# Kernel tuning notes

Measured on AMD Instinct MI355X. Metric: run time of the kernel, lower is better.

The kernel has to match this reference:

```python
import jax, jax.numpy as jnp
import numpy as np

N = 4096; TD = 768; ID = 512; H = 256; NH = 4; HD = H // NH; NC = 3; E = 131072


def _gcn(x, w, b, src, dst, n):
    # GCNConv: add self loops, sym-normalize, aggregate at dst
    loop = jnp.arange(n)
    s = jnp.concatenate([src, loop])
    d = jnp.concatenate([dst, loop])
    deg = jax.ops.segment_sum(jnp.ones(s.shape[0], x.dtype), d, num_segments=n)
    dinv = jnp.where(deg > 0, jax.lax.rsqrt(deg), 0.0)
    norm = dinv[s] * dinv[d]                      # [E+N]
    h = x @ w                                     # [N,H] transform
    out = jax.ops.segment_sum(norm[:, None] * h[s], d, num_segments=n)
    return out + b


def setup_inputs() -> dict:
    key = jax.random.key(0)
    ks = jax.random.split(key, 20)
    p = lambda k, shp, sc: jax.random.normal(k, shp, jnp.float32) * sc
    inp = {
        "text_features": jax.random.normal(ks[0], (N, TD), jnp.float32),
        "image_features": jax.random.normal(ks[1], (N, ID), jnp.float32),
        "edge_index": jax.random.randint(ks[2], (2, E), 0, N, jnp.int32),
        "text_w": p(ks[3], (TD, H), 0.02), "text_b": jnp.zeros((H,), jnp.float32),
        "image_w": p(ks[4], (ID, H), 0.02), "image_b": jnp.zeros((H,), jnp.float32),
        "wq": p(ks[5], (H, H), 0.02), "bq": jnp.zeros((H,), jnp.float32),
        "wk": p(ks[6], (H, H), 0.02), "bk": jnp.zeros((H,), jnp.float32),
        "wv": p(ks[7], (H, H), 0.02), "bv": jnp.zeros((H,), jnp.float32),
        "wo": p(ks[8], (H, H), 0.02), "bo": jnp.zeros((H,), jnp.float32),
        "gcn1_w": p(ks[9], (H, H), 0.02), "gcn1_b": jnp.zeros((H,), jnp.float32),
        "gcn2_w": p(ks[10], (H, H), 0.02), "gcn2_b": jnp.zeros((H,), jnp.float32),
        "cls_w": p(ks[11], (H, NC), 0.02), "cls_b": jnp.zeros((NC,), jnp.float32),
    }
    return inp


def reference(text_features, image_features, edge_index,
              text_w, text_b, image_w, image_b,
              wq, bq, wk, bk, wv, bv, wo, bo,
              gcn1_w, gcn1_b, gcn2_w, gcn2_b, cls_w, cls_b):
    # fused linear+relu projections, then elementwise fuse of sum
    combined = (jax.nn.relu(text_features @ text_w + text_b)
                + jax.nn.relu(image_features @ image_w + image_b))  # [N,H]
    # MHA over all nodes (seq_len=N, batch=1)
    q = (combined @ wq + bq).reshape(N, NH, HD)
    k = (combined @ wk + bk).reshape(N, NH, HD)
    v = (combined @ wv + bv).reshape(N, NH, HD)
    scores = jnp.einsum('nhd,mhd->hnm', q, k) / jnp.sqrt(jnp.float32(HD))
    attn = jax.nn.softmax(scores, axis=-1)
    o = jnp.einsum('hnm,mhd->nhd', attn, v).reshape(N, H)
    attn_out = o @ wo + bo
    # two GCN layers
    src, dst = edge_index[0], edge_index[1]
    g1 = jax.nn.relu(_gcn(attn_out, gcn1_w, gcn1_b, src, dst, N))
    g2 = _gcn(g1, gcn2_w, gcn2_b, src, dst, N)
    return g2 @ cls_w + cls_b
```

## Files before the change

kernel.cpp:

```cpp
#include <hip/hip_runtime.h>
#include <hip/hip_bf16.h>

typedef unsigned short ushort;
typedef __attribute__((ext_vector_type(8))) short short8;
typedef __attribute__((ext_vector_type(4))) short short4v;
typedef __attribute__((ext_vector_type(4))) float f32x4;

constexpr int N_  = 4096;
constexpr int TD_ = 768;
constexpr int ID_ = 512;
constexpr int H_  = 256;
constexpr int HD_ = 64;
constexpr int E_  = 131072;
constexpr int SPLITS = 8;
constexpr float QSCALE = 0.125f * 1.44269504088896f;

#define MFMA16(a, b, c) __builtin_amdgcn_mfma_f32_16x16x32_bf16(a, b, c, 0, 0, 0)

__device__ inline ushort f2bf(float x) {
    union { float f; unsigned u; } v; v.f = x;
    unsigned r = v.u + 0x7fff + ((v.u >> 16) & 1);
    return (ushort)(r >> 16);
}
__device__ inline float bf2f(ushort x) {
    union { unsigned u; float f; } v; v.u = ((unsigned)x) << 16;
    return v.f;
}

__device__ inline void gl_lds16(const void* g, void* l) {
    __builtin_amdgcn_global_load_lds((const __attribute__((address_space(1))) unsigned int*)g,
                                     (__attribute__((address_space(3))) unsigned int*)l, 16, 0, 0);
}

__device__ inline void stage64(const ushort* g, long long strideEl, ushort* lds, int w, int l) {
    int r8 = l >> 3;
    int cc = (l & 7) ^ r8;
    #pragma unroll
    for (int p = 0; p < 2; p++) {
        int row = w * 16 + p * 8 + r8;
        gl_lds16(g + (long long)row * strideEl + cc * 8, lds + (w * 16 + p * 8) * 64);
    }
}
__device__ inline int swz(int row, int kOff) {
    return row * 64 + ((((kOff >> 3) ^ (row & 7))) << 3);
}


__global__ __launch_bounds__(256) void k_init(int* __restrict__ indeg, int* __restrict__ pos) {
    int i = blockIdx.x * 256 + threadIdx.x;
    indeg[i] = 0;
    pos[i] = 0;
}

__global__ __launch_bounds__(256) void k_count(const int* __restrict__ dst, int* __restrict__ indeg) {
    int e = blockIdx.x * 256 + threadIdx.x;
    atomicAdd(&indeg[dst[e]], 1);
}

__global__ __launch_bounds__(1024) void k_scan(const int* __restrict__ indeg, int* __restrict__ offs,
                                               float* __restrict__ dinv) {
    __shared__ int sums[1024];
    int t = threadIdx.x;
    int b = t * 4;
    int a0 = indeg[b], a1 = indeg[b + 1], a2 = indeg[b + 2], a3 = indeg[b + 3];
    int s = a0 + a1 + a2 + a3;
    sums[t] = s;
    __syncthreads();
    for (int off = 1; off < 1024; off <<= 1) {
        int vv = (t >= off) ? sums[t - off] : 0;
        __syncthreads();
        sums[t] += vv;
        __syncthreads();
    }
    int excl = sums[t] - s;
    offs[b]     = excl;
    offs[b + 1] = excl + a0;
    offs[b + 2] = excl + a0 + a1;
    offs[b + 3] = excl + a0 + a1 + a2;
    dinv[b]     = 1.f / sqrtf((float)(a0 + 1));
    dinv[b + 1] = 1.f / sqrtf((float)(a1 + 1));
    dinv[b + 2] = 1.f / sqrtf((float)(a2 + 1));
    dinv[b + 3] = 1.f / sqrtf((float)(a3 + 1));
}

__global__ __launch_bounds__(256) void k_scatter(const int* __restrict__ src, const int* __restrict__ dst,
                                                 const int* __restrict__ offs, const float* __restrict__ dinv,
                                                 int* __restrict__ pos, int* __restrict__ ssrc,
                                                 float* __restrict__ sw) {
    int e = blockIdx.x * 256 + threadIdx.x;
    int s = src[e], d = dst[e];
    int p = atomicAdd(&pos[d], 1);
    int idx = offs[d] + p;
    ssrc[idx] = s;
    sw[idx] = dinv[s] * dinv[d];
}


__global__ __launch_bounds__(256) void k_cvt_feat(const float* __restrict__ text, const float* __restrict__ img,
                                                  ushort* __restrict__ tb, ushort* __restrict__ ib) {
    size_t base = ((size_t)blockIdx.x * 256 + threadIdx.x) * 8;
    const float* src;
    ushort* dst;
    if (base < (size_t)N_ * TD_) { src = text + base; dst = tb + base; }
    else { src = img + (base - (size_t)N_ * TD_); dst = ib + (base - (size_t)N_ * TD_); }
    float4 x = *(const float4*)src;
    float4 y = *(const float4*)(src + 4);
    ushort o[8] = { f2bf(x.x), f2bf(x.y), f2bf(x.z), f2bf(x.w),
                    f2bf(y.x), f2bf(y.y), f2bf(y.z), f2bf(y.w) };
    *(short8*)dst = *(const short8*)o;
}

__global__ __launch_bounds__(256) void k_cvtw(const float* __restrict__ tw, const float* __restrict__ iw,
                                              const float* __restrict__ wq, const float* __restrict__ wk,
                                              const float* __restrict__ wv, const float* __restrict__ wo,
                                              const float* __restrict__ g1w, const float* __restrict__ g2w,
                                              ushort* __restrict__ twT, ushort* __restrict__ iwT,
                                              ushort* __restrict__ wqT, ushort* __restrict__ wkT,
                                              ushort* __restrict__ wvT, ushort* __restrict__ woT,
                                              ushort* __restrict__ g1wT, ushort* __restrict__ g2wT) {
    __shared__ float Ts[64][65];
    const int zz = blockIdx.z;
    const float* src; ushort* dst; int R;
    switch (zz) {
        case 0: src = tw;  dst = twT;  R = 768; break;
        case 1: src = iw;  dst = iwT;  R = 512; break;
        case 2: src = wq;  dst = wqT;  R = 256; break;
        case 3: src = wk;  dst = wkT;  R = 256; break;
        case 4: src = wv;  dst = wvT;  R = 256; break;
        case 5: src = wo;  dst = woT;  R = 256; break;
        case 6: src = g1w; dst = g1wT; R = 256; break;
        default: src = g2w; dst = g2wT; R = 256; break;
    }
    const int r0 = blockIdx.x * 64, c0 = blockIdx.y * 64;
    if (r0 >= R) return;
    const int t = threadIdx.x;
    #pragma unroll
    for (int u = 0; u < 16; u++) {
        int lin = t + u * 256;
        int r = lin >> 6, c = lin & 63;
        Ts[r][c] = src[(size_t)(r0 + r) * 256 + c0 + c];
    }
    __syncthreads();
    #pragma unroll
    for (int u = 0; u < 16; u++) {
        int lin = t + u * 256;
        int c = lin >> 6, r = lin & 63;
        dst[(size_t)(c0 + c) * R + r0 + r] = f2bf(Ts[r][c]);
    }
}


__global__ __launch_bounds__(256) void k_combined_mfma(const ushort* __restrict__ text, const ushort* __restrict__ img,
                                                       const ushort* __restrict__ twT, const ushort* __restrict__ iwT,
                                                       const float* __restrict__ tb, const float* __restrict__ ib,
                                                       ushort* __restrict__ out) {
    __shared__ ushort As[2][64 * 64];
    __shared__ ushort Bs[2][64 * 64];
    __shared__ ushort Cs[64 * 72];
    const int bm = blockIdx.x * 64, bn = blockIdx.y * 64;
    const int t = threadIdx.x, w = t >> 6, l = t & 63, q = l >> 4, i = l & 15;
    constexpr int NCH = 20;

    auto stageC = [&](int c, int buf) {
        if (c < 12) {
            stage64(text + (size_t)bm * TD_ + c * 64, TD_, As[buf], w, l);
            stage64(twT + (size_t)bn * TD_ + c * 64, TD_, Bs[buf], w, l);
        } else {
            int cc = c - 12;
            stage64(img + (size_t)bm * ID_ + cc * 64, ID_, As[buf], w, l);
            stage64(iwT + (size_t)bn * ID_ + cc * 64, ID_, Bs[buf], w, l);
        }
    };

    f32x4 acc1[4], acc2[4];
    #pragma unroll
    for (int nt = 0; nt < 4; nt++) { acc1[nt] = (f32x4){0,0,0,0}; acc2[nt] = (f32x4){0,0,0,0}; }

    stageC(0, 0);
    for (int c = 0; c < NCH; c++) {
        __syncthreads();
        if (c + 1 < NCH) stageC(c + 1, (c + 1) & 1);
        const ushort* Ab = As[c & 1];
        const ushort* Bb = Bs[c & 1];
        f32x4* acc = (c < 12) ? acc1 : acc2;
        #pragma unroll
        for (int kb = 0; kb < 2; kb++) {
            short8 af = *(const short8*)&Ab[swz(w * 16 + i, kb * 32 + q * 8)];
            #pragma unroll
            for (int nt = 0; nt < 4; nt++) {
                short8 bfr = *(const short8*)&Bb[swz(nt * 16 + i, kb * 32 + q * 8)];
                acc[nt] = MFMA16(af, bfr, acc[nt]);
            }
        }
    }
    __syncthreads();
    #pragma unroll
    for (int nt = 0; nt < 4; nt++) {
        float b1 = tb[bn + nt * 16 + i], b2 = ib[bn + nt * 16 + i];
        #pragma unroll
        for (int r = 0; r < 4; r++) {
            float v = fmaxf(acc1[nt][r] + b1, 0.f) + fmaxf(acc2[nt][r] + b2, 0.f);
            Cs[(w * 16 + q * 4 + r) * 72 + nt * 16 + i] = f2bf(v);
        }
    }
    __syncthreads();
    int rr = t >> 2, c16 = (t & 3) * 16;
    short8 v0 = *(const short8*)&Cs[rr * 72 + c16];
    short8 v1 = *(const short8*)&Cs[rr * 72 + c16 + 8];
    ushort* dst = out + (size_t)(bm + rr) * H_ + bn + c16;
    *(short8*)dst = v0;
    *(short8*)(dst + 8) = v1;
}


__global__ __launch_bounds__(256) void k_qkv_mfma(const ushort* __restrict__ A,
                                                  const ushort* __restrict__ WqT, const ushort* __restrict__ WkT,
                                                  const ushort* __restrict__ WvT,
                                                  const float* __restrict__ bq, const float* __restrict__ bk,
                                                  const float* __restrict__ bv,
                                                  ushort* __restrict__ Qg, ushort* __restrict__ Kg,
                                                  ushort* __restrict__ Vtg) {
    __shared__ ushort As[2][64 * 64];
    __shared__ ushort Bs[2][64 * 64];
    __shared__ ushort Cs[64 * 72];
    const int bm = blockIdx.x * 64, head = blockIdx.y, z = blockIdx.z;
    const ushort* WT = (z == 0) ? WqT : (z == 1) ? WkT : WvT;
    const float* bias = (z == 0) ? bq : (z == 1) ? bk : bv;
    const int t = threadIdx.x, w = t >> 6, l = t & 63, q = l >> 4, i = l & 15;
    f32x4 acc[4];
    #pragma unroll
    for (int nt = 0; nt < 4; nt++) acc[nt] = (f32x4){0,0,0,0};

    auto stageC = [&](int c, int buf) {
        stage64(A + (size_t)bm * H_ + c * 64, H_, As[buf], w, l);
        stage64(WT + (size_t)(head * 64) * H_ + c * 64, H_, Bs[buf], w, l);
    };

    stageC(0, 0);
    for (int c = 0; c < 4; c++) {
        __syncthreads();
        if (c < 3) stageC(c + 1, (c + 1) & 1);
        const ushort* Ab = As[c & 1];
        const ushort* Bb = Bs[c & 1];
        #pragma unroll
        for (int kb = 0; kb < 2; kb++) {
            short8 af = *(const short8*)&Ab[swz(w * 16 + i, kb * 32 + q * 8)];
            #pragma unroll
            for (int nt = 0; nt < 4; nt++) {
                short8 bfr = *(const short8*)&Bb[swz(nt * 16 + i, kb * 32 + q * 8)];
                acc[nt] = MFMA16(af, bfr, acc[nt]);
            }
        }
    }
    __syncthreads();
    #pragma unroll
    for (int nt = 0; nt < 4; nt++) {
        float bv_ = bias[head * 64 + nt * 16 + i];
        #pragma unroll
        for (int r = 0; r < 4; r++) {
            float v = acc[nt][r] + bv_;
            if (z == 0) v *= QSCALE;
            if (z < 2) Cs[(w * 16 + q * 4 + r) * 72 + nt * 16 + i] = f2bf(v);
            else       Cs[(nt * 16 + i) * 72 + w * 16 + q * 4 + r] = f2bf(v);
        }
    }
    __syncthreads();
    int rr = t >> 2, c16 = (t & 3) * 16;
    short8 v0 = *(const short8*)&Cs[rr * 72 + c16];
    short8 v1 = *(const short8*)&Cs[rr * 72 + c16 + 8];
    ushort* dst;
    if (z < 2) dst = ((z == 0) ? Qg : Kg) + (size_t)head * N_ * HD_ + (size_t)(bm + rr) * HD_ + c16;
    else       dst = Vtg + (size_t)head * HD_ * N_ + (size_t)rr * N_ + bm + c16;
    *(short8*)dst = v0;
    *(short8*)(dst + 8) = v1;
}


__global__ __launch_bounds__(256) void k_attn_mfma(const ushort* __restrict__ Qg, const ushort* __restrict__ Kg,
                                                   const ushort* __restrict__ Vtg, ushort* __restrict__ Op,
                                                   float* __restrict__ lp) {
    __shared__ ushort Ks[64 * 64];
    __shared__ ushort Vs[64 * 64];
    __shared__ ushort Ps[4][16 * 72];
    const int head = blockIdx.y, r0 = blockIdx.x * 64, z = blockIdx.z;
    const int t = threadIdx.x, w = t >> 6, l = t & 63, q = l >> 4, i = l & 15;

    short8 qf[2];
    #pragma unroll
    for (int kb = 0; kb < 2; kb++)
        qf[kb] = *(const short8*)(Qg + ((size_t)head * N_ + r0 + w * 16 + i) * HD_ + kb * 32 + q * 8);

    f32x4 Oacc[4];
    float lacc[4];
    #pragma unroll
    for (int r = 0; r < 4; r++) { lacc[r] = 0.f; Oacc[r] = (f32x4){0,0,0,0}; }

    const int NT = 64 / SPLITS;
    for (int cb = z * NT; cb < z * NT + NT; cb++) {
        __syncthreads();
        stage64(Kg + ((size_t)head * N_ + cb * 64) * HD_, HD_, Ks, w, l);
        stage64(Vtg + (size_t)head * HD_ * N_ + cb * 64, N_, Vs, w, l);
        __syncthreads();

        f32x4 S[4];
        #pragma unroll
        for (int ct = 0; ct < 4; ct++) S[ct] = (f32x4){0,0,0,0};
        #pragma unroll
        for (int kb = 0; kb < 2; kb++) {
            #pragma unroll
            for (int ct = 0; ct < 4; ct++) {
                short8 kf = *(const short8*)&Ks[swz(ct * 16 + i, kb * 32 + q * 8)];
                S[ct] = MFMA16(qf[kb], kf, S[ct]);
            }
        }

        #pragma unroll
        for (int ct = 0; ct < 4; ct++) {
            #pragma unroll
            for (int r = 0; r < 4; r++) {
                float p = exp2f(S[ct][r]);
                lacc[r] += p;
                Ps[w][(q * 4 + r) * 72 + ct * 16 + i] = f2bf(p);
            }
        }
        #pragma unroll
        for (int kb = 0; kb < 2; kb++) {
            short8 pf = *(const short8*)&Ps[w][i * 72 + kb * 32 + q * 8];
            #pragma unroll
            for (int dt = 0; dt < 4; dt++) {
                short8 vf = *(const short8*)&Vs[swz(dt * 16 + i, kb * 32 + q * 8)];
                Oacc[dt] = MFMA16(pf, vf, Oacc[dt]);
            }
        }
    }

    #pragma unroll
    for (int off = 1; off < 16; off <<= 1)
        #pragma unroll
        for (int r = 0; r < 4; r++) lacc[r] += __shfl_xor(lacc[r], off);

    const size_t sh = ((size_t)z * 4 + head) * N_;
    #pragma unroll
    for (int r = 0; r < 4; r++) {
        int row = r0 + w * 16 + q * 4 + r;
        #pragma unroll
        for (int dt = 0; dt < 4; dt++)
            Op[(sh + row) * HD_ + dt * 16 + i] = f2bf(Oacc[dt][r]);
        if (i == 0) lp[sh + row] = lacc[r];
    }
}

__global__ __launch_bounds__(256) void k_attn_merge(const ushort* __restrict__ Op, const float* __restrict__ lp,
                                                    ushort* __restrict__ obuf) {
    const int t = threadIdx.x;
    const int idx = blockIdx.x * 16 + (t >> 4);
    const int h = idx >> 12, n = idx & 4095;
    const int d4 = (t & 15) * 4;
    float lsum = 0.f;
    float acc[4] = {0.f, 0.f, 0.f, 0.f};
    #pragma unroll
    for (int s = 0; s < SPLITS; s++) {
        size_t sh = ((size_t)s * 4 + h) * N_ + n;
        lsum += lp[sh];
        short4v o4 = *(const short4v*)&Op[sh * HD_ + d4];
        #pragma unroll
        for (int j = 0; j < 4; j++) acc[j] += bf2f((ushort)o4[j]);
    }
    float inv = 1.f / lsum;
    ushort res[4];
    #pragma unroll
    for (int j = 0; j < 4; j++) res[j] = f2bf(acc[j] * inv);
    *(short4v*)&obuf[(size_t)n * H_ + h * HD_ + d4] = *(const short4v*)res;
}


template <bool BIAS, bool RELU, bool BF16OUT>
__global__ __launch_bounds__(256) void k_gemm_bf16(const ushort* __restrict__ A, const ushort* __restrict__ BT,
                                                   const float* __restrict__ bias,
                                                   ushort* __restrict__ outb, float* __restrict__ outf) {
    __shared__ ushort As[2][64 * 64];
    __shared__ ushort Bs[2][64 * 64];
    __shared__ ushort Cs[64 * 72];
    const int bm = blockIdx.x * 64, bn = blockIdx.y * 64;
    const int t = threadIdx.x, w = t >> 6, l = t & 63, q = l >> 4, i = l & 15;
    f32x4 acc[4];
    #pragma unroll
    for (int nt = 0; nt < 4; nt++) acc[nt] = (f32x4){0,0,0,0};

    stage64(A + (size_t)bm * H_, H_, As[0], w, l);
    stage64(BT + (size_t)bn * H_, H_, Bs[0], w, l);
    for (int c = 0; c < 4; c++) {
        __syncthreads();
        if (c < 3) {
            stage64(A + (size_t)bm * H_ + (c + 1) * 64, H_, As[(c + 1) & 1], w, l);
            stage64(BT + (size_t)bn * H_ + (c + 1) * 64, H_, Bs[(c + 1) & 1], w, l);
        }
        const ushort* Ab = As[c & 1];
        const ushort* Bb = Bs[c & 1];
        #pragma unroll
        for (int kb = 0; kb < 2; kb++) {
            short8 af = *(const short8*)&Ab[swz(w * 16 + i, kb * 32 + q * 8)];
            #pragma unroll
            for (int nt = 0; nt < 4; nt++) {
                short8 bfr = *(const short8*)&Bb[swz(nt * 16 + i, kb * 32 + q * 8)];
                acc[nt] = MFMA16(af, bfr, acc[nt]);
            }
        }
    }
    if (BF16OUT) {
        __syncthreads();
        #pragma unroll
        for (int nt = 0; nt < 4; nt++) {
            float bb = BIAS ? bias[bn + nt * 16 + i] : 0.f;
            #pragma unroll
            for (int r = 0; r < 4; r++) {
                float v = acc[nt][r] + bb;
                if (RELU) v = fmaxf(v, 0.f);
                Cs[(w * 16 + q * 4 + r) * 72 + nt * 16 + i] = f2bf(v);
            }
        }
        __syncthreads();
        int rr = t >> 2, c16 = (t & 3) * 16;
        short8 v0 = *(const short8*)&Cs[rr * 72 + c16];
        short8 v1 = *(const short8*)&Cs[rr * 72 + c16 + 8];
        ushort* dst = outb + (size_t)(bm + rr) * H_ + bn + c16;
        *(short8*)dst = v0;
        *(short8*)(dst + 8) = v1;
    } else {
        #pragma unroll
        for (int nt = 0; nt < 4; nt++) {
            float bb = BIAS ? bias[bn + nt * 16 + i] : 0.f;
            #pragma unroll
            for (int r = 0; r < 4; r++) {
                float v = acc[nt][r] + bb;
                if (RELU) v = fmaxf(v, 0.f);
                outf[(size_t)(bm + w * 16 + q * 4 + r) * H_ + bn + nt * 16 + i] = v;
            }
        }
    }
}


template <bool RELU, bool BF16OUT>
__global__ __launch_bounds__(256) void k_agg(const ushort* __restrict__ h, const int* __restrict__ ssrc,
                                             const float* __restrict__ sw, const int* __restrict__ offs,
                                             const int* __restrict__ indeg, const float* __restrict__ dinv,
                                             const float* __restrict__ bias,
                                             ushort* __restrict__ outb, float* __restrict__ outf) {
    const int j = blockIdx.x;
    const int t = threadIdx.x;
    __shared__ int se[256];
    __shared__ float swt[256];
    float dj = dinv[j];
    float acc = dj * dj * bf2f(h[(size_t)j * H_ + t]);
    int start = offs[j], cnt = indeg[j];
    for (int base = 0; base < cnt; base += 256) {
        int m = cnt - base;
        if (m > 256) m = 256;
        __syncthreads();
        if (t < m) {
            se[t] = ssrc[start + base + t];
            swt[t] = sw[start + base + t];
        }
        __syncthreads();
        for (int i = 0; i < m; i++) acc += swt[i] * bf2f(h[(size_t)se[i] * H_ + t]);
    }
    acc += bias[t];
    if (RELU) acc = fmaxf(acc, 0.f);
    if (BF16OUT) outb[(size_t)j * H_ + t] = f2bf(acc);
    else         outf[(size_t)j * H_ + t] = acc;
}


__global__ __launch_bounds__(256) void k_cls(const float* __restrict__ x, const float* __restrict__ cw,
                                             const float* __restrict__ cb, float* __restrict__ out) {
    int row = blockIdx.x * 4 + (threadIdx.x >> 6);
    int lane = threadIdx.x & 63;
    const float* xr = x + (size_t)row * H_;
    float p0 = 0.f, p1 = 0.f, p2 = 0.f;
    #pragma unroll
    for (int kk = lane; kk < H_; kk += 64) {
        float xv = xr[kk];
        p0 += xv * cw[kk * 3 + 0];
        p1 += xv * cw[kk * 3 + 1];
        p2 += xv * cw[kk * 3 + 2];
    }
    #pragma unroll
    for (int off = 32; off > 0; off >>= 1) {
        p0 += __shfl_xor(p0, off);
        p1 += __shfl_xor(p1, off);
        p2 += __shfl_xor(p2, off);
    }
    if (lane == 0) {
        out[row * 3 + 0] = p0 + cb[0];
        out[row * 3 + 1] = p1 + cb[1];
        out[row * 3 + 2] = p2 + cb[2];
    }
}


extern "C" void kernel_launch(void* const* d_in, const int* in_sizes, int n_in,
                              void* d_out, int out_size, void* d_ws, size_t ws_size,
                              hipStream_t stream) {
    const float* text = (const float*)d_in[0];
    const float* img  = (const float*)d_in[1];
    const int*   eidx = (const int*)d_in[2];
    const float* tw  = (const float*)d_in[3];
    const float* tb  = (const float*)d_in[4];
    const float* iw  = (const float*)d_in[5];
    const float* ib  = (const float*)d_in[6];
    const float* wq  = (const float*)d_in[7];
    const float* bq  = (const float*)d_in[8];
    const float* wk  = (const float*)d_in[9];
    const float* bk  = (const float*)d_in[10];
    const float* wv  = (const float*)d_in[11];
    const float* bv  = (const float*)d_in[12];
    const float* wo  = (const float*)d_in[13];
    const float* bo  = (const float*)d_in[14];
    const float* g1w = (const float*)d_in[15];
    const float* g1b = (const float*)d_in[16];
    const float* g2w = (const float*)d_in[17];
    const float* g2b = (const float*)d_in[18];
    const float* cw  = (const float*)d_in[19];
    const float* cbv = (const float*)d_in[20];

    char* W = (char*)d_ws;
    size_t cur = 0;
    auto alloc = [&](size_t sz) { char* p = W + cur; cur += (sz + 255) & ~(size_t)255; return p; };

    float* dinv  = (float*)alloc(N_ * 4);
    float* swv   = (float*)alloc(E_ * 4);
    int* indeg   = (int*)alloc(N_ * 4);
    int* offs    = (int*)alloc(N_ * 4);
    int* pos     = (int*)alloc(N_ * 4);
    int* ssrc    = (int*)alloc(E_ * 4);
    ushort* Qg   = (ushort*)alloc((size_t)N_ * H_ * 2);
    ushort* Kg   = (ushort*)alloc((size_t)N_ * H_ * 2);
    ushort* Vtg  = (ushort*)alloc((size_t)N_ * H_ * 2);
    ushort* obuf = (ushort*)alloc((size_t)N_ * H_ * 2);
    ushort* woT  = (ushort*)alloc((size_t)H_ * H_ * 2);
    ushort* g1wT = (ushort*)alloc((size_t)H_ * H_ * 2);
    ushort* g2wT = (ushort*)alloc((size_t)H_ * H_ * 2);
    float* lp    = (float*)alloc((size_t)SPLITS * 4 * N_ * 4);
    char* S = W + cur;

    ushort* textbf = (ushort*)S;
    ushort* imgbf  = textbf + (size_t)N_ * TD_;
    ushort* twT    = imgbf + (size_t)N_ * ID_;
    ushort* iwT    = twT + (size_t)TD_ * H_;
    ushort* wqT    = iwT + (size_t)ID_ * H_;
    ushort* wkT    = wqT + (size_t)H_ * H_;
    ushort* wvT    = wkT + (size_t)H_ * H_;
    ushort* combbf = wvT + (size_t)H_ * H_;
    ushort* Op = (ushort*)S;
    ushort* attn_out = (ushort*)S;
    ushort* hbuf     = (ushort*)(S + (size_t)2 * 1024 * 1024);
    ushort* g1b16    = (ushort*)(S + (size_t)4 * 1024 * 1024);
    float* g2        = (float*)(S + (size_t)6 * 1024 * 1024);

    const int* esrc = eidx;
    const int* edst = eidx + E_;

    k_init<<<dim3(N_ / 256), dim3(256), 0, stream>>>(indeg, pos);
    k_count<<<dim3(E_ / 256), dim3(256), 0, stream>>>(edst, indeg);
    k_scan<<<dim3(1), dim3(1024), 0, stream>>>(indeg, offs, dinv);
    k_scatter<<<dim3(E_ / 256), dim3(256), 0, stream>>>(esrc, edst, offs, dinv, pos, ssrc, swv);

    k_cvt_feat<<<dim3((N_ * (TD_ + ID_)) / 2048), dim3(256), 0, stream>>>(text, img, textbf, imgbf);
    k_cvtw<<<dim3(12, 4, 8), dim3(256), 0, stream>>>(tw, iw, wq, wk, wv, wo, g1w, g2w,
                                                     twT, iwT, wqT, wkT, wvT, woT, g1wT, g2wT);

    k_combined_mfma<<<dim3(64, 4), dim3(256), 0, stream>>>(textbf, imgbf, twT, iwT, tb, ib, combbf);
    k_qkv_mfma<<<dim3(64, 4, 3), dim3(256), 0, stream>>>(combbf, wqT, wkT, wvT, bq, bk, bv, Qg, Kg, Vtg);
    k_attn_mfma<<<dim3(64, 4, SPLITS), dim3(256), 0, stream>>>(Qg, Kg, Vtg, Op, lp);
    k_attn_merge<<<dim3(1024), dim3(256), 0, stream>>>(Op, lp, obuf);

    k_gemm_bf16<true, false, true><<<dim3(64, 4), dim3(256), 0, stream>>>(obuf, woT, bo, attn_out, nullptr);
    k_gemm_bf16<false, false, true><<<dim3(64, 4), dim3(256), 0, stream>>>(attn_out, g1wT, nullptr, hbuf, nullptr);
    k_agg<true, true><<<dim3(N_), dim3(256), 0, stream>>>(hbuf, ssrc, swv, offs, indeg, dinv, g1b, g1b16, nullptr);
    k_gemm_bf16<false, false, true><<<dim3(64, 4), dim3(256), 0, stream>>>(g1b16, g2wT, nullptr, hbuf, nullptr);
    k_agg<false, false><<<dim3(N_), dim3(256), 0, stream>>>(hbuf, ssrc, swv, offs, indeg, dinv, g2b, nullptr, g2);

    k_cls<<<dim3(N_ / 4), dim3(256), 0, stream>>>(g2, cw, cbv, (float*)d_out);
}
```

Baseline: 254.3 us.

## Fold Wo into GCN1 weight, merge attention splits into GEMM, fuse agg with classifier

Several changes land together. The prep kernels are merged into one, and Wo is folded algebraically into the GCN1 weight through a small weight-product kernel. Attention splits drop from 8 to 4, the K/V tiles are double-buffered, and the P tile is written in a packed, swizzled form. The split merge and normalisation now happen inside the first GEMM's A-tile load, and the aggregation kernels use one wave per node with vectorised gathers, with the classifier fused into the final aggregation. The goal is fewer launches and fewer intermediate round trips through memory. The cost is an extra bf16 rounding of the folded weight.

```diff
diff --git a/kernel.cpp b/kernel.cpp
--- a/kernel.cpp
+++ b/kernel.cpp
@@ -3,7 +3,6 @@
 
 typedef unsigned short ushort;
 typedef __attribute__((ext_vector_type(8))) short short8;
-typedef __attribute__((ext_vector_type(4))) short short4v;
 typedef __attribute__((ext_vector_type(4))) float f32x4;
 
 constexpr int N_  = 4096;
@@ -12,7 +11,7 @@
 constexpr int H_  = 256;
 constexpr int HD_ = 64;
 constexpr int E_  = 131072;
-constexpr int SPLITS = 8;
+constexpr int SPLITS = 4;
 constexpr float QSCALE = 0.125f * 1.44269504088896f;
 
 #define MFMA16(a, b, c) __builtin_amdgcn_mfma_f32_16x16x32_bf16(a, b, c, 0, 0, 0)
@@ -22,10 +21,8 @@
     unsigned r = v.u + 0x7fff + ((v.u >> 16) & 1);
     return (ushort)(r >> 16);
 }
-__device__ inline float bf2f(ushort x) {
-    union { unsigned u; float f; } v; v.u = ((unsigned)x) << 16;
-    return v.f;
-}
+__device__ inline float lo2f(unsigned u) { union { unsigned x; float f; } v; v.x = u << 16; return v.f; }
+__device__ inline float hi2f(unsigned u) { union { unsigned x; float f; } v; v.x = u & 0xffff0000u; return v.f; }
 
 __device__ inline void gl_lds16(const void* g, void* l) {
     __builtin_amdgcn_global_load_lds((const __attribute__((address_space(1))) unsigned int*)g,
@@ -96,44 +93,44 @@
 }
 
 
-__global__ __launch_bounds__(256) void k_cvt_feat(const float* __restrict__ text, const float* __restrict__ img,
-                                                  ushort* __restrict__ tb, ushort* __restrict__ ib) {
-    size_t base = ((size_t)blockIdx.x * 256 + threadIdx.x) * 8;
-    const float* src;
-    ushort* dst;
-    if (base < (size_t)N_ * TD_) { src = text + base; dst = tb + base; }
-    else { src = img + (base - (size_t)N_ * TD_); dst = ib + (base - (size_t)N_ * TD_); }
-    float4 x = *(const float4*)src;
-    float4 y = *(const float4*)(src + 4);
-    ushort o[8] = { f2bf(x.x), f2bf(x.y), f2bf(x.z), f2bf(x.w),
-                    f2bf(y.x), f2bf(y.y), f2bf(y.z), f2bf(y.w) };
-    *(short8*)dst = *(const short8*)o;
-}
-
-__global__ __launch_bounds__(256) void k_cvtw(const float* __restrict__ tw, const float* __restrict__ iw,
+__global__ __launch_bounds__(256) void k_prep(const float* __restrict__ text, const float* __restrict__ img,
+                                              const float* __restrict__ tw, const float* __restrict__ iw,
                                               const float* __restrict__ wq, const float* __restrict__ wk,
                                               const float* __restrict__ wv, const float* __restrict__ wo,
                                               const float* __restrict__ g1w, const float* __restrict__ g2w,
+                                              ushort* __restrict__ textbf, ushort* __restrict__ imgbf,
+                                              ushort* __restrict__ wobf,
                                               ushort* __restrict__ twT, ushort* __restrict__ iwT,
                                               ushort* __restrict__ wqT, ushort* __restrict__ wkT,
-                                              ushort* __restrict__ wvT, ushort* __restrict__ woT,
-                                              ushort* __restrict__ g1wT, ushort* __restrict__ g2wT) {
+                                              ushort* __restrict__ wvT, ushort* __restrict__ g1wT,
+                                              ushort* __restrict__ g2wT) {
     __shared__ float Ts[64][65];
-    const int zz = blockIdx.z;
-    const float* src; ushort* dst; int R;
-    switch (zz) {
-        case 0: src = tw;  dst = twT;  R = 768; break;
-        case 1: src = iw;  dst = iwT;  R = 512; break;
-        case 2: src = wq;  dst = wqT;  R = 256; break;
-        case 3: src = wk;  dst = wkT;  R = 256; break;
-        case 4: src = wv;  dst = wvT;  R = 256; break;
-        case 5: src = wo;  dst = woT;  R = 256; break;
-        case 6: src = g1w; dst = g1wT; R = 256; break;
-        default: src = g2w; dst = g2wT; R = 256; break;
-    }
-    const int r0 = blockIdx.x * 64, c0 = blockIdx.y * 64;
-    if (r0 >= R) return;
+    const int b = blockIdx.x;
     const int t = threadIdx.x;
+    if (b < 2592) {
+        size_t base = ((size_t)b * 256 + t) * 8;
+        const size_t TXE = (size_t)N_ * TD_, IME = (size_t)N_ * ID_;
+        const float* src; ushort* dst;
+        if (base < TXE) { src = text + base; dst = textbf + base; }
+        else if (base < TXE + IME) { src = img + (base - TXE); dst = imgbf + (base - TXE); }
+        else { src = wo + (base - TXE - IME); dst = wobf + (base - TXE - IME); }
+        float4 x = *(const float4*)src;
+        float4 y = *(const float4*)(src + 4);
+        ushort o[8] = { f2bf(x.x), f2bf(x.y), f2bf(x.z), f2bf(x.w),
+                        f2bf(y.x), f2bf(y.y), f2bf(y.z), f2bf(y.w) };
+        *(short8*)dst = *(const short8*)o;
+        return;
+    }
+    int wb = b - 2592;
+    const float* src; ushort* dst; int R, tile;
+    if (wb < 48)       { src = tw;  dst = twT;  R = 768; tile = wb; }
+    else if (wb < 80)  { src = iw;  dst = iwT;  R = 512; tile = wb - 48; }
+    else if (wb < 96)  { src = wq;  dst = wqT;  R = 256; tile = wb - 80; }
+    else if (wb < 112) { src = wk;  dst = wkT;  R = 256; tile = wb - 96; }
+    else if (wb < 128) { src = wv;  dst = wvT;  R = 256; tile = wb - 112; }
+    else if (wb < 144) { src = g1w; dst = g1wT; R = 256; tile = wb - 128; }
+    else               { src = g2w; dst = g2wT; R = 256; tile = wb - 144; }
+    const int r0 = (tile >> 2) * 64, c0 = (tile & 3) * 64;
     #pragma unroll
     for (int u = 0; u < 16; u++) {
         int lin = t + u * 256;
@@ -147,6 +144,64 @@
         int c = lin >> 6, r = lin & 63;
         dst[(size_t)(c0 + c) * R + r0 + r] = f2bf(Ts[r][c]);
     }
+}
+
+
+__global__ __launch_bounds__(256) void k_foldw(const ushort* __restrict__ g1wT, const ushort* __restrict__ wobf,
+                                               const float* __restrict__ bo,
+                                               ushort* __restrict__ WpT, float* __restrict__ bp) {
+    __shared__ ushort As[2][4096];
+    __shared__ ushort Bs[2][4096];
+    __shared__ ushort Cs[64 * 72];
+    const int t = threadIdx.x;
+    if (blockIdx.x == 16) {
+        float acc = 0.f;
+        const ushort* row = g1wT + (size_t)t * 256;
+        for (int m8 = 0; m8 < 256; m8 += 8) {
+            #pragma unroll
+            for (int j = 0; j < 8; j++) acc += bo[m8 + j] * lo2f(((unsigned)row[m8 + j]) << 16);
+        }
+        bp[t] = acc;
+        return;
+    }
+    const int bm = (blockIdx.x >> 2) * 64, bn = (blockIdx.x & 3) * 64;
+    const int w = t >> 6, l = t & 63, q = l >> 4, i = l & 15;
+    f32x4 acc[4];
+    #pragma unroll
+    for (int nt = 0; nt < 4; nt++) acc[nt] = (f32x4){0, 0, 0, 0};
+    stage64(g1wT + (size_t)bm * H_, H_, As[0], w, l);
+    stage64(wobf + (size_t)bn * H_, H_, Bs[0], w, l);
+    for (int c = 0; c < 4; c++) {
+        __syncthreads();
+        if (c < 3) {
+            stage64(g1wT + (size_t)bm * H_ + (c + 1) * 64, H_, As[(c + 1) & 1], w, l);
+            stage64(wobf + (size_t)bn * H_ + (c + 1) * 64, H_, Bs[(c + 1) & 1], w, l);
+        }
+        const ushort* Ab = As[c & 1];
+        const ushort* Bb = Bs[c & 1];
+        #pragma unroll
+        for (int kb = 0; kb < 2; kb++) {
+            short8 af = *(const short8*)&Ab[swz(w * 16 + i, kb * 32 + q * 8)];
+            #pragma unroll
+            for (int nt = 0; nt < 4; nt++) {
+                short8 bfr = *(const short8*)&Bb[swz(nt * 16 + i, kb * 32 + q * 8)];
+                acc[nt] = MFMA16(af, bfr, acc[nt]);
+            }
+        }
+    }
+    __syncthreads();
+    #pragma unroll
+    for (int nt = 0; nt < 4; nt++)
+        #pragma unroll
+        for (int r = 0; r < 4; r++)
+            Cs[(w * 16 + q * 4 + r) * 72 + nt * 16 + i] = f2bf(acc[nt][r]);
+    __syncthreads();
+    int rr = t >> 2, c16 = (t & 3) * 16;
+    short8 v0 = *(const short8*)&Cs[rr * 72 + c16];
+    short8 v1 = *(const short8*)&Cs[rr * 72 + c16 + 8];
+    ushort* dst = WpT + (size_t)(bm + rr) * H_ + bn + c16;
+    *(short8*)dst = v0;
+    *(short8*)(dst + 8) = v1;
 }
 
 
@@ -231,15 +286,14 @@
     #pragma unroll
     for (int nt = 0; nt < 4; nt++) acc[nt] = (f32x4){0,0,0,0};
 
-    auto stageC = [&](int c, int buf) {
-        stage64(A + (size_t)bm * H_ + c * 64, H_, As[buf], w, l);
-        stage64(WT + (size_t)(head * 64) * H_ + c * 64, H_, Bs[buf], w, l);
-    };
-
-    stageC(0, 0);
+    stage64(A + (size_t)bm * H_, H_, As[0], w, l);
+    stage64(WT + (size_t)(head * 64) * H_, H_, Bs[0], w, l);
     for (int c = 0; c < 4; c++) {
         __syncthreads();
-        if (c < 3) stageC(c + 1, (c + 1) & 1);
+        if (c < 3) {
+            stage64(A + (size_t)bm * H_ + (c + 1) * 64, H_, As[(c + 1) & 1], w, l);
+            stage64(WT + (size_t)(head * 64) * H_ + (c + 1) * 64, H_, Bs[(c + 1) & 1], w, l);
+        }
         const ushort* Ab = As[c & 1];
         const ushort* Bb = Bs[c & 1];
         #pragma unroll
@@ -279,11 +333,13 @@
 __global__ __launch_bounds__(256) void k_attn_mfma(const ushort* __restrict__ Qg, const ushort* __restrict__ Kg,
                                                    const ushort* __restrict__ Vtg, ushort* __restrict__ Op,
                                                    float* __restrict__ lp) {
-    __shared__ ushort Ks[64 * 64];
-    __shared__ ushort Vs[64 * 64];
+    __shared__ ushort Ks[2][4096];
+    __shared__ ushort Vs[2][4096];
     __shared__ ushort Ps[4][16 * 72];
     const int head = blockIdx.y, r0 = blockIdx.x * 64, z = blockIdx.z;
     const int t = threadIdx.x, w = t >> 6, l = t & 63, q = l >> 4, i = l & 15;
+    const int x3 = i & 3;
+    ushort* Pw = &Ps[w][0];
 
     short8 qf[2];
     #pragma unroll
@@ -291,101 +347,175 @@
         qf[kb] = *(const short8*)(Qg + ((size_t)head * N_ + r0 + w * 16 + i) * HD_ + kb * 32 + q * 8);
 
     f32x4 Oacc[4];
-    float lacc[4];
-    #pragma unroll
-    for (int r = 0; r < 4; r++) { lacc[r] = 0.f; Oacc[r] = (f32x4){0,0,0,0}; }
+    float lacc = 0.f;
+    #pragma unroll
+    for (int dt = 0; dt < 4; dt++) Oacc[dt] = (f32x4){0, 0, 0, 0};
 
     const int NT = 64 / SPLITS;
-    for (int cb = z * NT; cb < z * NT + NT; cb++) {
+    const int cb0 = z * NT;
+    stage64(Kg + ((size_t)head * N_ + (size_t)cb0 * 64) * HD_, HD_, Ks[0], w, l);
+    stage64(Vtg + (size_t)head * HD_ * N_ + cb0 * 64, N_, Vs[0], w, l);
+
+    for (int it = 0; it < NT; it++) {
         __syncthreads();
-        stage64(Kg + ((size_t)head * N_ + cb * 64) * HD_, HD_, Ks, w, l);
-        stage64(Vtg + (size_t)head * HD_ * N_ + cb * 64, N_, Vs, w, l);
+        if (it + 1 < NT) {
+            int cb = cb0 + it + 1;
+            stage64(Kg + ((size_t)head * N_ + (size_t)cb * 64) * HD_, HD_, Ks[(it + 1) & 1], w, l);
+            stage64(Vtg + (size_t)head * HD_ * N_ + cb * 64, N_, Vs[(it + 1) & 1], w, l);
+        }
+        const ushort* Kb = Ks[it & 1];
+        const ushort* Vb = Vs[it & 1];
+
+        f32x4 St[4];
+        #pragma unroll
+        for (int kt = 0; kt < 4; kt++) St[kt] = (f32x4){0, 0, 0, 0};
+        #pragma unroll
+        for (int kb = 0; kb < 2; kb++) {
+            #pragma unroll
+            for (int kt = 0; kt < 4; kt++) {
+                short8 kf = *(const short8*)&Kb[swz(kt * 16 + i, kb * 32 + q * 8)];
+                St[kt] = MFMA16(kf, qf[kb], St[kt]);
+            }
+        }
+
+        float ts = 0.f;
+        #pragma unroll
+        for (int kt = 0; kt < 4; kt++) {
+            float p0 = exp2f(St[kt][0]), p1 = exp2f(St[kt][1]);
+            float p2 = exp2f(St[kt][2]), p3 = exp2f(St[kt][3]);
+            ts += (p0 + p1) + (p2 + p3);
+            unsigned a = (unsigned)f2bf(p0) | ((unsigned)f2bf(p1) << 16);
+            unsigned b = (unsigned)f2bf(p2) | ((unsigned)f2bf(p3) << 16);
+            int off = i * 72 + (((2 * kt + (q >> 1)) ^ x3) << 3) + ((q & 1) << 2);
+            uint2 v; v.x = a; v.y = b;
+            *(uint2*)&Pw[off] = v;
+        }
+        lacc += ts;
+
+        #pragma unroll
+        for (int kb = 0; kb < 2; kb++) {
+            short8 pf = *(const short8*)&Pw[i * 72 + (((4 * kb + q) ^ x3) << 3)];
+            #pragma unroll
+            for (int dt = 0; dt < 4; dt++) {
+                short8 vf = *(const short8*)&Vb[swz(dt * 16 + i, kb * 32 + q * 8)];
+                Oacc[dt] = MFMA16(vf, pf, Oacc[dt]);
+            }
+        }
+    }
+
+    lacc += __shfl_xor(lacc, 16);
+    lacc += __shfl_xor(lacc, 32);
+
+    const size_t sh = ((size_t)z * 4 + head) * N_;
+    const int row = r0 + w * 16 + i;
+    #pragma unroll
+    for (int dt = 0; dt < 4; dt++) {
+        unsigned w0 = (unsigned)f2bf(Oacc[dt][0]) | ((unsigned)f2bf(Oacc[dt][1]) << 16);
+        unsigned w1 = (unsigned)f2bf(Oacc[dt][2]) | ((unsigned)f2bf(Oacc[dt][3]) << 16);
+        uint2 v; v.x = w0; v.y = w1;
+        *(uint2*)&Op[(sh + row) * HD_ + dt * 16 + q * 4] = v;
+    }
+    if (l < 16) lp[sh + r0 + w * 16 + l] = lacc;
+}
+
+
+__global__ __launch_bounds__(256) void k_gemm_merged(const ushort* __restrict__ Op, const float* __restrict__ lp,
+                                                     const ushort* __restrict__ WpT, const float* __restrict__ bp,
+                                                     ushort* __restrict__ outb) {
+    __shared__ ushort As[2][4096];
+    __shared__ ushort Bs[2][4096];
+    __shared__ ushort Cs[64 * 72];
+    const int bm = blockIdx.x * 64, bn = blockIdx.y * 64;
+    const int t = threadIdx.x, w = t >> 6, l = t & 63, q = l >> 4, i = l & 15;
+    const int rr = t >> 2, u2 = t & 3;
+
+    uint4 pre[8];
+    float lpre[4];
+    auto prefA = [&](int c) {
+        #pragma unroll
+        for (int s = 0; s < 4; s++) {
+            const ushort* p = Op + (((size_t)(s * 4 + c) * N_ + bm + rr) * HD_ + u2 * 16);
+            pre[s * 2]     = *(const uint4*)p;
+            pre[s * 2 + 1] = *(const uint4*)(p + 8);
+            lpre[s] = lp[(size_t)(s * 4 + c) * N_ + bm + rr];
+        }
+    };
+    ushort pk[16];
+    auto process = [&]() {
+        float inv = 1.f / (lpre[0] + lpre[1] + lpre[2] + lpre[3]);
+        float f[16];
+        #pragma unroll
+        for (int d = 0; d < 16; d++) f[d] = 0.f;
+        #pragma unroll
+        for (int s = 0; s < 4; s++) {
+            const unsigned* u = (const unsigned*)&pre[s * 2];
+            #pragma unroll
+            for (int d2 = 0; d2 < 8; d2++) {
+                f[d2 * 2]     += lo2f(u[d2]);
+                f[d2 * 2 + 1] += hi2f(u[d2]);
+            }
+        }
+        #pragma unroll
+        for (int d = 0; d < 16; d++) pk[d] = f2bf(f[d] * inv);
+    };
+
+    f32x4 acc[4];
+    #pragma unroll
+    for (int nt = 0; nt < 4; nt++) acc[nt] = (f32x4){0, 0, 0, 0};
+
+    prefA(0);
+    stage64(WpT + (size_t)bn * H_, H_, Bs[0], w, l);
+    process();
+    for (int c = 0; c < 4; c++) {
+        int u0 = u2 * 2;
+        *(short8*)&As[c & 1][rr * 64 + ((u0 ^ (rr & 7)) << 3)]       = *(const short8*)&pk[0];
+        *(short8*)&As[c & 1][rr * 64 + (((u0 + 1) ^ (rr & 7)) << 3)] = *(const short8*)&pk[8];
         __syncthreads();
-
-        f32x4 S[4];
-        #pragma unroll
-        for (int ct = 0; ct < 4; ct++) S[ct] = (f32x4){0,0,0,0};
+        if (c + 1 < 4) {
+            prefA(c + 1);
+            stage64(WpT + (size_t)bn * H_ + (c + 1) * 64, H_, Bs[(c + 1) & 1], w, l);
+        }
+        const ushort* Ab = As[c & 1];
+        const ushort* Bb = Bs[c & 1];
         #pragma unroll
         for (int kb = 0; kb < 2; kb++) {
-            #pragma unroll
-            for (int ct = 0; ct < 4; ct++) {
-                short8 kf = *(const short8*)&Ks[swz(ct * 16 + i, kb * 32 + q * 8)];
-                S[ct] = MFMA16(qf[kb], kf, S[ct]);
+            short8 af = *(const short8*)&Ab[swz(w * 16 + i, kb * 32 + q * 8)];
+            #pragma unroll
+            for (int nt = 0; nt < 4; nt++) {
+                short8 bfr = *(const short8*)&Bb[swz(nt * 16 + i, kb * 32 + q * 8)];
+                acc[nt] = MFMA16(af, bfr, acc[nt]);
             }
         }
-
-        #pragma unroll
-        for (int ct = 0; ct < 4; ct++) {
-            #pragma unroll
-            for (int r = 0; r < 4; r++) {
-                float p = exp2f(S[ct][r]);
-                lacc[r] += p;
-                Ps[w][(q * 4 + r) * 72 + ct * 16 + i] = f2bf(p);
-            }
-        }
-        #pragma unroll
-        for (int kb = 0; kb < 2; kb++) {
-            short8 pf = *(const short8*)&Ps[w][i * 72 + kb * 32 + q * 8];
-            #pragma unroll
-            for (int dt = 0; dt < 4; dt++) {
-                short8 vf = *(const short8*)&Vs[swz(dt * 16 + i, kb * 32 + q * 8)];
-                Oacc[dt] = MFMA16(pf, vf, Oacc[dt]);
-            }
-        }
-    }
-
-    #pragma unroll
-    for (int off = 1; off < 16; off <<= 1)
-        #pragma unroll
-        for (int r = 0; r < 4; r++) lacc[r] += __shfl_xor(lacc[r], off);
-
-    const size_t sh = ((size_t)z * 4 + head) * N_;
-    #pragma unroll
-    for (int r = 0; r < 4; r++) {
-        int row = r0 + w * 16 + q * 4 + r;
-        #pragma unroll
-        for (int dt = 0; dt < 4; dt++)
-            Op[(sh + row) * HD_ + dt * 16 + i] = f2bf(Oacc[dt][r]);
-        if (i == 0) lp[sh + row] = lacc[r];
-    }
-}
-
-__global__ __launch_bounds__(256) void k_attn_merge(const ushort* __restrict__ Op, const float* __restrict__ lp,
-                                                    ushort* __restrict__ obuf) {
-    const int t = threadIdx.x;
-    const int idx = blockIdx.x * 16 + (t >> 4);
-    const int h = idx >> 12, n = idx & 4095;
-    const int d4 = (t & 15) * 4;
-    float lsum = 0.f;
-    float acc[4] = {0.f, 0.f, 0.f, 0.f};
-    #pragma unroll
-    for (int s = 0; s < SPLITS; s++) {
-        size_t sh = ((size_t)s * 4 + h) * N_ + n;
-        lsum += lp[sh];
-        short4v o4 = *(const short4v*)&Op[sh * HD_ + d4];
-        #pragma unroll
-        for (int j = 0; j < 4; j++) acc[j] += bf2f((ushort)o4[j]);
-    }
-    float inv = 1.f / lsum;
-    ushort res[4];
-    #pragma unroll
-    for (int j = 0; j < 4; j++) res[j] = f2bf(acc[j] * inv);
-    *(short4v*)&obuf[(size_t)n * H_ + h * HD_ + d4] = *(const short4v*)res;
-}
-
-
-template <bool BIAS, bool RELU, bool BF16OUT>
+        if (c + 1 < 4) process();
+    }
+    __syncthreads();
+    #pragma unroll
+    for (int nt = 0; nt < 4; nt++) {
+        float bb = bp[bn + nt * 16 + i];
+        #pragma unroll
+        for (int r = 0; r < 4; r++)
+            Cs[(w * 16 + q * 4 + r) * 72 + nt * 16 + i] = f2bf(acc[nt][r] + bb);
+    }
+    __syncthreads();
+    int c16 = (t & 3) * 16;
+    short8 v0 = *(const short8*)&Cs[rr * 72 + c16];
+    short8 v1 = *(const short8*)&Cs[rr * 72 + c16 + 8];
+    ushort* dst = outb + (size_t)(bm + rr) * H_ + bn + c16;
+    *(short8*)dst = v0;
+    *(short8*)(dst + 8) = v1;
+}
+
+
 __global__ __launch_bounds__(256) void k_gemm_bf16(const ushort* __restrict__ A, const ushort* __restrict__ BT,
-                                                   const float* __restrict__ bias,
-                                                   ushort* __restrict__ outb, float* __restrict__ outf) {
-    __shared__ ushort As[2][64 * 64];
-    __shared__ ushort Bs[2][64 * 64];
+                                                   ushort* __restrict__ outb) {
+    __shared__ ushort As[2][4096];
+    __shared__ ushort Bs[2][4096];
     __shared__ ushort Cs[64 * 72];
     const int bm = blockIdx.x * 64, bn = blockIdx.y * 64;
     const int t = threadIdx.x, w = t >> 6, l = t & 63, q = l >> 4, i = l & 15;
     f32x4 acc[4];
     #pragma unroll
-    for (int nt = 0; nt < 4; nt++) acc[nt] = (f32x4){0,0,0,0};
+    for (int nt = 0; nt < 4; nt++) acc[nt] = (f32x4){0, 0, 0, 0};
 
     stage64(A + (size_t)bm * H_, H_, As[0], w, l);
     stage64(BT + (size_t)bn * H_, H_, Bs[0], w, l);
@@ -407,83 +537,81 @@
             }
         }
     }
-    if (BF16OUT) {
-        __syncthreads();
-        #pragma unroll
-        for (int nt = 0; nt < 4; nt++) {
-            float bb = BIAS ? bias[bn + nt * 16 + i] : 0.f;
-            #pragma unroll
-            for (int r = 0; r < 4; r++) {
-                float v = acc[nt][r] + bb;
-                if (RELU) v = fmaxf(v, 0.f);
-                Cs[(w * 16 + q * 4 + r) * 72 + nt * 16 + i] = f2bf(v);
-            }
-        }
-        __syncthreads();
-        int rr = t >> 2, c16 = (t & 3) * 16;
-        short8 v0 = *(const short8*)&Cs[rr * 72 + c16];
-        short8 v1 = *(const short8*)&Cs[rr * 72 + c16 + 8];
-        ushort* dst = outb + (size_t)(bm + rr) * H_ + bn + c16;
-        *(short8*)dst = v0;
-        *(short8*)(dst + 8) = v1;
-    } else {
-        #pragma unroll
-        for (int nt = 0; nt < 4; nt++) {
-            float bb = BIAS ? bias[bn + nt * 16 + i] : 0.f;
-            #pragma unroll
-            for (int r = 0; r < 4; r++) {
-                float v = acc[nt][r] + bb;
-                if (RELU) v = fmaxf(v, 0.f);
-                outf[(size_t)(bm + w * 16 + q * 4 + r) * H_ + bn + nt * 16 + i] = v;
-            }
-        }
-    }
-}
-
-
-template <bool RELU, bool BF16OUT>
-__global__ __launch_bounds__(256) void k_agg(const ushort* __restrict__ h, const int* __restrict__ ssrc,
-                                             const float* __restrict__ sw, const int* __restrict__ offs,
-                                             const int* __restrict__ indeg, const float* __restrict__ dinv,
-                                             const float* __restrict__ bias,
-                                             ushort* __restrict__ outb, float* __restrict__ outf) {
-    const int j = blockIdx.x;
+    __syncthreads();
+    #pragma unroll
+    for (int nt = 0; nt < 4; nt++)
+        #pragma unroll
+        for (int r = 0; r < 4; r++)
+            Cs[(w * 16 + q * 4 + r) * 72 + nt * 16 + i] = f2bf(acc[nt][r]);
+    __syncthreads();
+    int rr = t >> 2, c16 = (t & 3) * 16;
+    short8 v0 = *(const short8*)&Cs[rr * 72 + c16];
+    short8 v1 = *(const short8*)&Cs[rr * 72 + c16 + 8];
+    ushort* dst = outb + (size_t)(bm + rr) * H_ + bn + c16;
+    *(short8*)dst = v0;
+    *(short8*)(dst + 8) = v1;
+}
+
+
+__global__ __launch_bounds__(256) void k_agg1(const ushort* __restrict__ h, const int* __restrict__ ssrc,
+                                              const float* __restrict__ sw, const int* __restrict__ offs,
+                                              const int* __restrict__ indeg, const float* __restrict__ dinv,
+                                              const float* __restrict__ bias, ushort* __restrict__ outb) {
     const int t = threadIdx.x;
-    __shared__ int se[256];
-    __shared__ float swt[256];
+    const int j = blockIdx.x * 4 + (t >> 6);
+    const int d0 = (t & 63) * 4;
     float dj = dinv[j];
-    float acc = dj * dj * bf2f(h[(size_t)j * H_ + t]);
+    uint2 hv = *(const uint2*)&h[(size_t)j * H_ + d0];
+    float s2 = dj * dj;
+    float a0 = s2 * lo2f(hv.x), a1 = s2 * hi2f(hv.x), a2 = s2 * lo2f(hv.y), a3 = s2 * hi2f(hv.y);
     int start = offs[j], cnt = indeg[j];
-    for (int base = 0; base < cnt; base += 256) {
-        int m = cnt - base;
-        if (m > 256) m = 256;
-        __syncthreads();
-        if (t < m) {
-            se[t] = ssrc[start + base + t];
-            swt[t] = sw[start + base + t];
-        }
-        __syncthreads();
-        for (int i = 0; i < m; i++) acc += swt[i] * bf2f(h[(size_t)se[i] * H_ + t]);
-    }
-    acc += bias[t];
-    if (RELU) acc = fmaxf(acc, 0.f);
-    if (BF16OUT) outb[(size_t)j * H_ + t] = f2bf(acc);
-    else         outf[(size_t)j * H_ + t] = acc;
-}
-
-
-__global__ __launch_bounds__(256) void k_cls(const float* __restrict__ x, const float* __restrict__ cw,
-                                             const float* __restrict__ cb, float* __restrict__ out) {
-    int row = blockIdx.x * 4 + (threadIdx.x >> 6);
-    int lane = threadIdx.x & 63;
-    const float* xr = x + (size_t)row * H_;
+    for (int e = 0; e < cnt; e++) {
+        int s = ssrc[start + e];
+        float wg = sw[start + e];
+        uint2 v = *(const uint2*)&h[(size_t)s * H_ + d0];
+        a0 += wg * lo2f(v.x); a1 += wg * hi2f(v.x);
+        a2 += wg * lo2f(v.y); a3 += wg * hi2f(v.y);
+    }
+    a0 = fmaxf(a0 + bias[d0], 0.f);
+    a1 = fmaxf(a1 + bias[d0 + 1], 0.f);
+    a2 = fmaxf(a2 + bias[d0 + 2], 0.f);
+    a3 = fmaxf(a3 + bias[d0 + 3], 0.f);
+    uint2 o;
+    o.x = (unsigned)f2bf(a0) | ((unsigned)f2bf(a1) << 16);
+    o.y = (unsigned)f2bf(a2) | ((unsigned)f2bf(a3) << 16);
+    *(uint2*)&outb[(size_t)j * H_ + d0] = o;
+}
+
+
+__global__ __launch_bounds__(256) void k_aggcls(const ushort* __restrict__ h, const int* __restrict__ ssrc,
+                                                const float* __restrict__ sw, const int* __restrict__ offs,
+                                                const int* __restrict__ indeg, const float* __restrict__ dinv,
+                                                const float* __restrict__ bias, const float* __restrict__ cw,
+                                                const float* __restrict__ cb, float* __restrict__ out) {
+    const int t = threadIdx.x;
+    const int j = blockIdx.x * 4 + (t >> 6);
+    const int lane = t & 63;
+    const int d0 = lane * 4;
+    float dj = dinv[j];
+    uint2 hv = *(const uint2*)&h[(size_t)j * H_ + d0];
+    float s2 = dj * dj;
+    float a0 = s2 * lo2f(hv.x), a1 = s2 * hi2f(hv.x), a2 = s2 * lo2f(hv.y), a3 = s2 * hi2f(hv.y);
+    int start = offs[j], cnt = indeg[j];
+    for (int e = 0; e < cnt; e++) {
+        int s = ssrc[start + e];
+        float wg = sw[start + e];
+        uint2 v = *(const uint2*)&h[(size_t)s * H_ + d0];
+        a0 += wg * lo2f(v.x); a1 += wg * hi2f(v.x);
+        a2 += wg * lo2f(v.y); a3 += wg * hi2f(v.y);
+    }
+    a0 += bias[d0]; a1 += bias[d0 + 1]; a2 += bias[d0 + 2]; a3 += bias[d0 + 3];
     float p0 = 0.f, p1 = 0.f, p2 = 0.f;
     #pragma unroll
-    for (int kk = lane; kk < H_; kk += 64) {
-        float xv = xr[kk];
-        p0 += xv * cw[kk * 3 + 0];
-        p1 += xv * cw[kk * 3 + 1];
-        p2 += xv * cw[kk * 3 + 2];
+    for (int r = 0; r < 4; r++) {
+        float g = (r == 0) ? a0 : (r == 1) ? a1 : (r == 2) ? a2 : a3;
+        p0 += g * cw[(d0 + r) * 3 + 0];
+        p1 += g * cw[(d0 + r) * 3 + 1];
+        p2 += g * cw[(d0 + r) * 3 + 2];
     }
     #pragma unroll
     for (int off = 32; off > 0; off >>= 1) {
@@ -492,9 +620,9 @@
         p2 += __shfl_xor(p2, off);
     }
     if (lane == 0) {
-        out[row * 3 + 0] = p0 + cb[0];
-        out[row * 3 + 1] = p1 + cb[1];
-        out[row * 3 + 2] = p2 + cb[2];
+        out[j * 3 + 0] = p0 + cb[0];
+        out[j * 3 + 1] = p1 + cb[1];
+        out[j * 3 + 2] = p2 + cb[2];
     }
 }
 
@@ -537,10 +665,11 @@
     ushort* Qg   = (ushort*)alloc((size_t)N_ * H_ * 2);
     ushort* Kg   = (ushort*)alloc((size_t)N_ * H_ * 2);
     ushort* Vtg  = (ushort*)alloc((size_t)N_ * H_ * 2);
-    ushort* obuf = (ushort*)alloc((size_t)N_ * H_ * 2);
-    ushort* woT  = (ushort*)alloc((size_t)H_ * H_ * 2);
+    ushort* WpT  = (ushort*)alloc((size_t)H_ * H_ * 2);
+    float* bp    = (float*)alloc(H_ * 4);
     ushort* g1wT = (ushort*)alloc((size_t)H_ * H_ * 2);
     ushort* g2wT = (ushort*)alloc((size_t)H_ * H_ * 2);
+    ushort* wobf = (ushort*)alloc((size_t)H_ * H_ * 2);
     float* lp    = (float*)alloc((size_t)SPLITS * 4 * N_ * 4);
     char* S = W + cur;
 
@@ -553,10 +682,9 @@
     ushort* wvT    = wkT + (size_t)H_ * H_;
     ushort* combbf = wvT + (size_t)H_ * H_;
     ushort* Op = (ushort*)S;
-    ushort* attn_out = (ushort*)S;
-    ushort* hbuf     = (ushort*)(S + (size_t)2 * 1024 * 1024);
-    ushort* g1b16    = (ushort*)(S + (size_t)4 * 1024 * 1024);
-    float* g2        = (float*)(S + (size_t)6 * 1024 * 1024);
+    ushort* hbuf  = (ushort*)(S + (size_t)4 * 1024 * 1024);
+    ushort* g1b16 = (ushort*)(S + (size_t)6 * 1024 * 1024);
+    ushort* hbuf2 = (ushort*)(S + (size_t)8 * 1024 * 1024);
 
     const int* esrc = eidx;
     const int* edst = eidx + E_;
@@ -566,20 +694,17 @@
     k_scan<<<dim3(1), dim3(1024), 0, stream>>>(indeg, offs, dinv);
     k_scatter<<<dim3(E_ / 256), dim3(256), 0, stream>>>(esrc, edst, offs, dinv, pos, ssrc, swv);
 
-    k_cvt_feat<<<dim3((N_ * (TD_ + ID_)) / 2048), dim3(256), 0, stream>>>(text, img, textbf, imgbf);
-    k_cvtw<<<dim3(12, 4, 8), dim3(256), 0, stream>>>(tw, iw, wq, wk, wv, wo, g1w, g2w,
-                                                     twT, iwT, wqT, wkT, wvT, woT, g1wT, g2wT);
+    k_prep<<<dim3(2752), dim3(256), 0, stream>>>(text, img, tw, iw, wq, wk, wv, wo, g1w, g2w,
+                                                 textbf, imgbf, wobf, twT, iwT, wqT, wkT, wvT, g1wT, g2wT);
+    k_foldw<<<dim3(17), dim3(256), 0, stream>>>(g1wT, wobf, bo, WpT, bp);
 
     k_combined_mfma<<<dim3(64, 4), dim3(256), 0, stream>>>(textbf, imgbf, twT, iwT, tb, ib, combbf);
     k_qkv_mfma<<<dim3(64, 4, 3), dim3(256), 0, stream>>>(combbf, wqT, wkT, wvT, bq, bk, bv, Qg, Kg, Vtg);
     k_attn_mfma<<<dim3(64, 4, SPLITS), dim3(256), 0, stream>>>(Qg, Kg, Vtg, Op, lp);
-    k_attn_merge<<<dim3(1024), dim3(256), 0, stream>>>(Op, lp, obuf);
-
-    k_gemm_bf16<true, false, true><<<dim3(64, 4), dim3(256), 0, stream>>>(obuf, woT, bo, attn_out, nullptr);
-    k_gemm_bf16<false, false, true><<<dim3(64, 4), dim3(256), 0, stream>>>(attn_out, g1wT, nullptr, hbuf, nullptr);
-    k_agg<true, true><<<dim3(N_), dim3(256), 0, stream>>>(hbuf, ssrc, swv, offs, indeg, dinv, g1b, g1b16, nullptr);
-    k_gemm_bf16<false, false, true><<<dim3(64, 4), dim3(256), 0, stream>>>(g1b16, g2wT, nullptr, hbuf, nullptr);
-    k_agg<false, false><<<dim3(N_), dim3(256), 0, stream>>>(hbuf, ssrc, swv, offs, indeg, dinv, g2b, nullptr, g2);
-
-    k_cls<<<dim3(N_ / 4), dim3(256), 0, stream>>>(g2, cw, cbv, (float*)d_out);
-}
+
+    k_gemm_merged<<<dim3(64, 4), dim3(256), 0, stream>>>(Op, lp, WpT, bp, hbuf);
+    k_agg1<<<dim3(N_ / 4), dim3(256), 0, stream>>>(hbuf, ssrc, swv, offs, indeg, dinv, g1b, g1b16);
+    k_gemm_bf16<<<dim3(64, 4), dim3(256), 0, stream>>>(g1b16, g2wT, hbuf2);
+    k_aggcls<<<dim3(N_ / 4), dim3(256), 0, stream>>>(hbuf2, ssrc, swv, offs, indeg, dinv, g2b, cw, cbv,
+                                                     (float*)d_out);
+}
```

Result: slower. 272.4 us (+7.1%).
